# Kernel optimization log

Measured on AMD Instinct MI355X. Metric: run time of the kernel, lower is better.

## Reference

```python
import jax, jax.numpy as jnp
import numpy as np

K = 512           # num_embeddings
D = 256           # embedding_dim
GRID = (16, 32)   # SOM grid, prod == K
SIGMA = 2.0       # Gaussian neighborhood width (blur at step 0)
COMMITMENT_COST = 0.25
KOHONEN_COST = 1.0


def _make_blur_matrix():
    # Grid.init id->coord: coord[j] = (i // prod(shape[:j])) % shape[j]
    idx = np.arange(K)
    c0 = idx % GRID[0]
    c1 = (idx // GRID[0]) % GRID[1]
    coords = np.stack([c0, c1], axis=-1).astype(np.float32)  # [K, 2]
    dist = np.linalg.norm(coords[None, :, :] - coords[:, None, :], axis=-1)  # [K, K]
    return jnp.asarray(np.exp(-(dist ** 2) / (2.0 * SIGMA ** 2)), dtype=jnp.float32)


def setup_inputs() -> dict:
    key = jax.random.key(0)
    kx, kw = jax.random.split(key)
    x = jax.random.normal(kx, (64, 32, 32, D), dtype=jnp.float32)
    w = jax.random.normal(kw, (K, D), dtype=jnp.float32)
    bmat = _make_blur_matrix()  # [K, K] constant buffer
    return {"x": x, "w": w, "bmat": bmat}


def reference(x, w, bmat):
    sg = jax.lax.stop_gradient
    flat = x.reshape(-1, D)  # [N, D]

    # nearest-code search (no_grad in torch)
    fw = sg(flat)
    ww = sg(w)
    dists = (jnp.sum(fw ** 2, axis=1, keepdims=True)
             + jnp.sum(ww ** 2, axis=1)
             - 2.0 * fw @ ww.T)                       # [N, K]
    enc_idx = jnp.argmin(dists, axis=1)               # [N]
    encodings = jax.nn.one_hot(enc_idx, K, dtype=jnp.float32)  # [N, K]

    # embedding lookup (differentiable w.r.t. w)
    quant_flat = w[enc_idx]                           # [N, D]
    quantized = quant_flat.reshape(x.shape)

    # l2_batch(w, quantized.detach()) -> [N, K]
    qd = sg(quant_flat)
    diff = (jnp.sum(w ** 2, axis=1)[None, :]
            + jnp.sum(qd ** 2, axis=1, keepdims=True)
            - 2.0 * qd @ w.T)                         # [N, K]

    # blur-weighted kohonen loss: bmm(diff[N,1,K], bmat[idx][N,K,1]).mean()
    selected = bmat[enc_idx]                          # [N, K]
    kohonen_loss = jnp.mean(jnp.sum(diff * selected, axis=-1))

    avg_probs = jnp.mean(encodings, axis=0)
    perplexity = jnp.exp(-jnp.sum(avg_probs * jnp.log(avg_probs + 1e-10)))

    e_latent = jnp.mean((sg(quantized) - x) ** 2)
    q_latent = jnp.mean((quantized - sg(x)) ** 2)
    loss = q_latent + COMMITMENT_COST * e_latent + KOHONEN_COST * kohonen_loss

    quantized_st = x + sg(quantized - x)              # straight-through
    return loss, quantized_st, perplexity, enc_idx
```

## Files before the change

### kernel.cpp

```cpp
#include <hip/hip_runtime.h>
#include <hip/hip_bf16.h>
#include <hip/hip_fp16.h>
#include <math.h>

#define NPTS 65536
#define DIM  256
#define KC   512

#define BM    64
#define NTILE 4
#define NBLK  256
#define XSTR  264
#define EPS   0.01f

#define QOFF  1
#define PIDX  16777217
#define EOFF  16777218


typedef _Float16 h8    __attribute__((ext_vector_type(8)));
typedef float    f32x4 __attribute__((ext_vector_type(4)));

__device__ inline void cvt_split8(float4 a, float4 b, h8& hv, h8& lv) {
    float f[8] = {a.x, a.y, a.z, a.w, b.x, b.y, b.z, b.w};
    #pragma unroll
    for (int i = 0; i < 8; ++i) {
        _Float16 h = (_Float16)f[i];
        hv[i] = h;
        lv[i] = (_Float16)(f[i] - (float)h);
    }
}

__device__ inline void merge_top2(float& b1, int& i1, float& b2, int& i2,
                                  float ob1, int oi1, float ob2, int oi2) {
    bool ow = (ob1 < b1) || (ob1 == b1 && oi1 < i1);
    float lb = ow ? b1 : ob1; int li = ow ? i1 : oi1;
    if (ow) { b1 = ob1; i1 = oi1; }
    float c2 = b2; int ci = i2;
    if (ob2 < c2 || (ob2 == c2 && oi2 < ci)) { c2 = ob2; ci = oi2; }
    if (lb  < c2 || (lb  == c2 && li  < ci)) { c2 = lb;  ci = li;  }
    b2 = c2; i2 = ci;
}

__device__ inline float exact_dist(const float* __restrict__ xr,
                                   const float* __restrict__ w, int c, float wsqc) {
    const float* wr = w + (size_t)c * DIM;
    float d0 = 0.f, d1 = 0.f, d2 = 0.f, d3 = 0.f;
    #pragma unroll 4
    for (int d = 0; d < DIM; d += 4) {
        d0 = fmaf(xr[d + 0], wr[d + 0], d0);
        d1 = fmaf(xr[d + 1], wr[d + 1], d1);
        d2 = fmaf(xr[d + 2], wr[d + 2], d2);
        d3 = fmaf(xr[d + 3], wr[d + 3], d3);
    }
    return wsqc - 2.f * ((d0 + d1) + (d2 + d3));
}

__global__ __launch_bounds__(256) void som_wsq(const float* __restrict__ w,
                                               float* __restrict__ wsq,
                                               int* __restrict__ hist,
                                               double* __restrict__ mse_acc)
{
    int k = blockIdx.x * 256 + threadIdx.x;
    const float4* r = reinterpret_cast<const float4*>(w + (size_t)k * DIM);
    float s0 = 0.f, s1 = 0.f, s2 = 0.f, s3 = 0.f;
    #pragma unroll 8
    for (int q = 0; q < DIM / 4; ++q) {
        float4 v = r[q];
        s0 = fmaf(v.x, v.x, s0);
        s1 = fmaf(v.y, v.y, s1);
        s2 = fmaf(v.z, v.z, s2);
        s3 = fmaf(v.w, v.w, s3);
    }
    wsq[k] = (s0 + s1) + (s2 + s3);
    hist[k] = 0;
    if (k == 0) *mse_acc = 0.0;
}

__global__ __launch_bounds__(256) void som_conv(const float* __restrict__ w,
                                                _Float16* __restrict__ wfh,
                                                _Float16* __restrict__ wfl)
{
    const int tid = threadIdx.x;
    const int row = blockIdx.x * 8 + (tid >> 5);
    const int g   = tid & 31;
    const float4* r = reinterpret_cast<const float4*>(w + (size_t)row * DIM);
    float4 a = r[g * 2], b = r[g * 2 + 1];
    h8 hv, lv; cvt_split8(a, b, hv, lv);
    int dsl = g >> 2, kg = g & 3;
    int ctg = row >> 4, l15 = row & 15;
    size_t off = (((size_t)(ctg * 8 + dsl)) * 4 + kg) * 128 + l15 * 8;
    *reinterpret_cast<h8*>(wfh + off) = hv;
    *reinterpret_cast<h8*>(wfl + off) = lv;
}

__global__ __launch_bounds__(512) void som_main(const float* __restrict__ x,
                                                const float* __restrict__ w,
                                                const _Float16* __restrict__ wfh,
                                                const _Float16* __restrict__ wfl,
                                                float* __restrict__ out,
                                                const float* __restrict__ wsq,
                                                int* __restrict__ hist,
                                                double* __restrict__ mse_acc)
{
    alignas(16) __shared__ _Float16 xh[2][BM * XSTR];
    alignas(16) __shared__ _Float16 xl[2][BM * XSTR];
    __shared__ float wsq_s[KC];
    __shared__ float xsq_s[2][BM];
    __shared__ float red_b[8][BM], red_s[8][BM];
    __shared__ int   red_ib[8][BM], red_is[8][BM];
    __shared__ int   bidx_s[BM];

    const int tid  = threadIdx.x;
    const int lane = tid & 63;
    const int wid  = tid >> 6;
    const int l15  = lane & 15;
    const int kg   = lane >> 4;
    const int tile0 = blockIdx.x * NTILE;

    wsq_s[tid] = wsq[tid];

    const float4* xg4 = reinterpret_cast<const float4*>(x);
    const float4* wg4 = reinterpret_cast<const float4*>(w);
    float4* q4 = reinterpret_cast<float4*>(out + QOFF);

    float4 xr[4][2];

    auto loadx = [&](int tt) {
        #pragma unroll
        for (int it = 0; it < 4; ++it) {
            int u = it * 512 + tid, row = u >> 5, c8 = u & 31;
            size_t base = (size_t)(tt * BM + row) * 64 + c8 * 2;
            xr[it][0] = xg4[base];
            xr[it][1] = xg4[base + 1];
        }
    };
    auto cvtwrite = [&](int c) {
        #pragma unroll
        for (int it = 0; it < 4; ++it) {
            int u = it * 512 + tid, row = u >> 5, c8 = u & 31;
            h8 hv, lv; cvt_split8(xr[it][0], xr[it][1], hv, lv);
            *reinterpret_cast<h8*>(&xh[c][row * XSTR + c8 * 8]) = hv;
            *reinterpret_cast<h8*>(&xl[c][row * XSTR + c8 * 8]) = lv;
            float4 a = xr[it][0], b = xr[it][1];
            float s = ((fmaf(a.x, a.x, a.y * a.y) + fmaf(a.z, a.z, a.w * a.w))
                     + (fmaf(b.x, b.x, b.y * b.y) + fmaf(b.z, b.z, b.w * b.w)));
            #pragma unroll
            for (int m = 1; m <= 16; m <<= 1) s += __shfl_xor(s, m, 64);
            if ((lane & 31) == 0) xsq_s[c][row] = s;
        }
    };

    loadx(tile0);
    cvtwrite(0);
    loadx(tile0 + 1);
    __syncthreads();

    const int codeBase = wid * 64;
    const int ctg0 = codeBase >> 4;
    const _Float16* __restrict__ pH = wfh + kg * 128 + l15 * 8;
    const _Float16* __restrict__ pL = wfl + kg * 128 + l15 * 8;

    #pragma unroll 1
    for (int t = 0; t < NTILE; ++t) {
        const int c = t & 1;
        const int ptBlock = (tile0 + t) * BM;
        const _Float16* __restrict__ bxh = xh[c];
        const _Float16* __restrict__ bxl = xl[c];

        f32x4 acc[4][4];
        #pragma unroll
        for (int rt = 0; rt < 4; ++rt)
            #pragma unroll
            for (int ct = 0; ct < 4; ++ct)
                acc[rt][ct] = (f32x4){0.f, 0.f, 0.f, 0.f};

        #pragma unroll 1
        for (int dsl = 0; dsl < 8; ++dsl) {
            h8 Bh[4], Bl[4];
            #pragma unroll
            for (int ct = 0; ct < 4; ++ct) {
                int boff = (ct * 16 + l15) * XSTR + dsl * 32 + kg * 8;
                Bh[ct] = *reinterpret_cast<const h8*>(&bxh[boff]);
                Bl[ct] = *reinterpret_cast<const h8*>(&bxl[boff]);
            }
            #pragma unroll
            for (int rt = 0; rt < 4; ++rt) {
                size_t aoff = ((size_t)((ctg0 + rt) * 8 + dsl)) * 512;
                h8 Ah = *reinterpret_cast<const h8*>(pH + aoff);
                h8 Al = *reinterpret_cast<const h8*>(pL + aoff);
                #pragma unroll
                for (int ct = 0; ct < 4; ++ct)
                    acc[rt][ct] = __builtin_amdgcn_mfma_f32_16x16x32_f16(Ah, Bh[ct], acc[rt][ct], 0, 0, 0);
                #pragma unroll
                for (int ct = 0; ct < 4; ++ct)
                    acc[rt][ct] = __builtin_amdgcn_mfma_f32_16x16x32_f16(Al, Bh[ct], acc[rt][ct], 0, 0, 0);
                #pragma unroll
                for (int ct = 0; ct < 4; ++ct)
                    acc[rt][ct] = __builtin_amdgcn_mfma_f32_16x16x32_f16(Ah, Bl[ct], acc[rt][ct], 0, 0, 0);
            }
        }

        float sb[4], ss[4];
        int   ib[4], is2[4];
        #pragma unroll
        for (int ct = 0; ct < 4; ++ct) { sb[ct] = INFINITY; ss[ct] = INFINITY; ib[ct] = 0; is2[ct] = 0; }
        #pragma unroll
        for (int rt = 0; rt < 4; ++rt) {
            int cbase = codeBase + rt * 16 + kg * 4;
            #pragma unroll
            for (int ct = 0; ct < 4; ++ct) {
                #pragma unroll
                for (int r = 0; r < 4; ++r) {
                    int cc = cbase + r;
                    float d = wsq_s[cc] - 2.f * acc[rt][ct][r];
                    if (d < sb[ct] || (d == sb[ct] && cc < ib[ct])) {
                        ss[ct] = sb[ct]; is2[ct] = ib[ct]; sb[ct] = d; ib[ct] = cc;
                    } else if (d < ss[ct] || (d == ss[ct] && cc < is2[ct])) {
                        ss[ct] = d; is2[ct] = cc;
                    }
                }
            }
        }
        #pragma unroll
        for (int ct = 0; ct < 4; ++ct) {
            #pragma unroll
            for (int m = 16; m <= 32; m <<= 1) {
                float ob1 = __shfl_xor(sb[ct], m, 64), ob2 = __shfl_xor(ss[ct], m, 64);
                int   oi1 = __shfl_xor(ib[ct], m, 64), oi2 = __shfl_xor(is2[ct], m, 64);
                merge_top2(sb[ct], ib[ct], ss[ct], is2[ct], ob1, oi1, ob2, oi2);
            }
        }
        if (kg == 0) {
            #pragma unroll
            for (int ct = 0; ct < 4; ++ct) {
                int p = ct * 16 + l15;
                red_b[wid][p] = sb[ct];  red_s[wid][p] = ss[ct];
                red_ib[wid][p] = ib[ct]; red_is[wid][p] = is2[ct];
            }
        }
        __syncthreads();

        if (tid < BM) {
            float b = red_b[0][tid], s = red_s[0][tid];
            int  bi = red_ib[0][tid], si = red_is[0][tid];
            #pragma unroll
            for (int g = 1; g < 8; ++g)
                merge_top2(b, bi, s, si, red_b[g][tid], red_ib[g][tid], red_s[g][tid], red_is[g][tid]);

            if (s - b < EPS) {
                const float* xrp = x + (size_t)(ptBlock + tid) * DIM;
                float d1 = exact_dist(xrp, w, bi, wsq_s[bi]);
                float d2 = exact_dist(xrp, w, si, wsq_s[si]);
                if (d2 < d1 || (d2 == d1 && si < bi)) { bi = si; b = d2; } else { b = d1; }
            }
            bidx_s[tid] = bi;
            out[EOFF + ptBlock + tid] = (float)bi;
            atomicAdd(&hist[bi], 1);

            float msum = xsq_s[c][tid] + b;
            #pragma unroll
            for (int m = 32; m; m >>= 1) msum += __shfl_xor(msum, m, 64);
            if (tid == 0) atomicAdd(mse_acc, (double)msum);
        }
        __syncthreads();

        #pragma unroll
        for (int r8 = 0; r8 < 8; ++r8) {
            int row = r8 * 8 + wid;
            int cc = bidx_s[row];
            q4[(size_t)(ptBlock + row) * 64 + lane] = wg4[(size_t)cc * 64 + lane];
        }
        if (t + 1 < NTILE) cvtwrite(c ^ 1);
        if (t + 2 < NTILE) loadx(tile0 + t + 2);
        __syncthreads();
    }
}

__global__ __launch_bounds__(256) void som_g(const float* __restrict__ w,
                                             const float* __restrict__ bmat,
                                             const float* __restrict__ wsq,
                                             float* __restrict__ g)
{
    __shared__ float wj[DIM];
    __shared__ float psum[4];
    const int j = blockIdx.x;
    const int tid = threadIdx.x;
    wj[tid] = w[(size_t)j * DIM + tid];
    __syncthreads();
    const float wsqj = wsq[j];
    float sum = 0.f;
    for (int k = tid; k < KC; k += 256) {
        const float* wk = &w[(size_t)k * DIM];
        float d0 = 0.f, d1 = 0.f, d2 = 0.f, d3 = 0.f;
        #pragma unroll 4
        for (int d = 0; d < DIM; d += 4) {
            d0 = fmaf(wj[d + 0], wk[d + 0], d0);
            d1 = fmaf(wj[d + 1], wk[d + 1], d1);
            d2 = fmaf(wj[d + 2], wk[d + 2], d2);
            d3 = fmaf(wj[d + 3], wk[d + 3], d3);
        }
        float dot = (d0 + d1) + (d2 + d3);
        float t = wsq[k] + wsqj - 2.f * dot;
        sum = fmaf(bmat[(size_t)j * KC + k], t, sum);
    }
    #pragma unroll
    for (int m = 32; m; m >>= 1) sum += __shfl_xor(sum, m, 64);
    int lane = tid & 63, wid = tid >> 6;
    if (lane == 0) psum[wid] = sum;
    __syncthreads();
    if (tid == 0) g[j] = (psum[0] + psum[1]) + (psum[2] + psum[3]);
}

__global__ __launch_bounds__(512) void som_final(const int* __restrict__ hist,
                                                 const float* __restrict__ g,
                                                 const double* __restrict__ mse_acc,
                                                 float* __restrict__ out)
{
    __shared__ float e_part[8], k_part[8];
    const int tid = threadIdx.x;
    int cnt = hist[tid];
    float p = (float)cnt / (float)NPTS;
    float ent = -p * logf(p + 1e-10f);
    float koh = (float)cnt * g[tid];
    #pragma unroll
    for (int m = 32; m; m >>= 1) {
        ent += __shfl_xor(ent, m, 64);
        koh += __shfl_xor(koh, m, 64);
    }
    int lane = tid & 63, wid = tid >> 6;
    if (lane == 0) { e_part[wid] = ent; k_part[wid] = koh; }
    __syncthreads();
    if (tid == 0) {
        float es = 0.f, ks = 0.f;
        #pragma unroll
        for (int i = 0; i < 8; ++i) { es += e_part[i]; ks += k_part[i]; }
        float mse = (float)(*mse_acc / (double)(NPTS * (size_t)DIM));
        out[0] = fmaf(1.25f, mse, ks / (float)NPTS);
        out[PIDX] = expf(es);
    }
}

extern "C" void kernel_launch(void* const* d_in, const int* in_sizes, int n_in,
                              void* d_out, int out_size, void* d_ws, size_t ws_size,
                              hipStream_t stream) {
    const float* x    = (const float*)d_in[0];
    const float* w    = (const float*)d_in[1];
    const float* bmat = (const float*)d_in[2];
    float* out = (float*)d_out;

    _Float16* wfh = (_Float16*)d_ws;
    _Float16* wfl = wfh + 131072;
    float*  wsq  = (float*)((char*)d_ws + 524288);
    float*  g    = (float*)((char*)d_ws + 526336);
    int*    hist = (int*)((char*)d_ws + 528384);
    double* mse  = (double*)((char*)d_ws + 530432);

    som_wsq  <<<2, 256, 0, stream>>>(w, wsq, hist, mse);
    som_conv <<<64, 256, 0, stream>>>(w, wfh, wfl);
    som_main <<<NBLK, 512, 0, stream>>>(x, w, wfh, wfl, out, wsq, hist, mse);
    som_g    <<<KC, 256, 0, stream>>>(w, bmat, wsq, g);
    som_final<<<1, KC, 0, stream>>>(hist, g, mse, out);
}
```

Baseline: 182.1 us.

## Use single fp16 MFMA pass with full exact rescan for ambiguous points

Drops the split hi/lo fp16 compensation, cutting the MFMA distance GEMM from three passes to one and halving the converted-weight buffers. Points whose top-two margin falls below a widened threshold are queued and rescanned exactly in fp32 against all 512 codes, one wave per flagged point. It also merges the wsq and conversion kernels into one, and assigns one tile per block (1024 blocks) instead of double-buffered four-tile blocks. The risk is that many flagged points make the serial full-codebook rescan expensive, and the coarser fp16 distances could miss true nearest codes outside the margin.

After: 457.9 us. 151% more time.

```diff
diff --git a/kernel.cpp b/kernel.cpp
--- a/kernel.cpp
+++ b/kernel.cpp
@@ -8,10 +8,9 @@
 #define KC   512
 
 #define BM    64
-#define NTILE 4
-#define NBLK  256
+#define NBLK  (NPTS / BM)
 #define XSTR  264
-#define EPS   0.01f
+#define EPS   0.1f
 
 #define QOFF  1
 #define PIDX  16777217
@@ -20,16 +19,6 @@
 
 typedef _Float16 h8    __attribute__((ext_vector_type(8)));
 typedef float    f32x4 __attribute__((ext_vector_type(4)));
-
-__device__ inline void cvt_split8(float4 a, float4 b, h8& hv, h8& lv) {
-    float f[8] = {a.x, a.y, a.z, a.w, b.x, b.y, b.z, b.w};
-    #pragma unroll
-    for (int i = 0; i < 8; ++i) {
-        _Float16 h = (_Float16)f[i];
-        hv[i] = h;
-        lv[i] = (_Float16)(f[i] - (float)h);
-    }
-}
 
 __device__ inline void merge_top2(float& b1, int& i1, float& b2, int& i2,
                                   float ob1, int oi1, float ob2, int oi2) {
@@ -42,238 +31,207 @@
     b2 = c2; i2 = ci;
 }
 
-__device__ inline float exact_dist(const float* __restrict__ xr,
-                                   const float* __restrict__ w, int c, float wsqc) {
-    const float* wr = w + (size_t)c * DIM;
-    float d0 = 0.f, d1 = 0.f, d2 = 0.f, d3 = 0.f;
+__global__ __launch_bounds__(256) void som_prep(const float* __restrict__ w,
+                                                _Float16* __restrict__ wfh,
+                                                float* __restrict__ wsq,
+                                                int* __restrict__ hist,
+                                                double* __restrict__ mse_acc)
+{
+    int c = blockIdx.x * 256 + threadIdx.x;
+    const float4* r = reinterpret_cast<const float4*>(w + (size_t)c * DIM);
+    float s0 = 0.f, s1 = 0.f, s2 = 0.f, s3 = 0.f;
     #pragma unroll 4
-    for (int d = 0; d < DIM; d += 4) {
-        d0 = fmaf(xr[d + 0], wr[d + 0], d0);
-        d1 = fmaf(xr[d + 1], wr[d + 1], d1);
-        d2 = fmaf(xr[d + 2], wr[d + 2], d2);
-        d3 = fmaf(xr[d + 3], wr[d + 3], d3);
-    }
-    return wsqc - 2.f * ((d0 + d1) + (d2 + d3));
-}
-
-__global__ __launch_bounds__(256) void som_wsq(const float* __restrict__ w,
-                                               float* __restrict__ wsq,
-                                               int* __restrict__ hist,
-                                               double* __restrict__ mse_acc)
-{
-    int k = blockIdx.x * 256 + threadIdx.x;
-    const float4* r = reinterpret_cast<const float4*>(w + (size_t)k * DIM);
-    float s0 = 0.f, s1 = 0.f, s2 = 0.f, s3 = 0.f;
-    #pragma unroll 8
-    for (int q = 0; q < DIM / 4; ++q) {
-        float4 v = r[q];
-        s0 = fmaf(v.x, v.x, s0);
-        s1 = fmaf(v.y, v.y, s1);
-        s2 = fmaf(v.z, v.z, s2);
-        s3 = fmaf(v.w, v.w, s3);
-    }
-    wsq[k] = (s0 + s1) + (s2 + s3);
-    hist[k] = 0;
-    if (k == 0) *mse_acc = 0.0;
-}
-
-__global__ __launch_bounds__(256) void som_conv(const float* __restrict__ w,
-                                                _Float16* __restrict__ wfh,
-                                                _Float16* __restrict__ wfl)
-{
-    const int tid = threadIdx.x;
-    const int row = blockIdx.x * 8 + (tid >> 5);
-    const int g   = tid & 31;
-    const float4* r = reinterpret_cast<const float4*>(w + (size_t)row * DIM);
-    float4 a = r[g * 2], b = r[g * 2 + 1];
-    h8 hv, lv; cvt_split8(a, b, hv, lv);
-    int dsl = g >> 2, kg = g & 3;
-    int ctg = row >> 4, l15 = row & 15;
-    size_t off = (((size_t)(ctg * 8 + dsl)) * 4 + kg) * 128 + l15 * 8;
-    *reinterpret_cast<h8*>(wfh + off) = hv;
-    *reinterpret_cast<h8*>(wfl + off) = lv;
+    for (int g = 0; g < 32; ++g) {
+        float4 a = r[g * 2], b = r[g * 2 + 1];
+        s0 = fmaf(a.x, a.x, s0); s1 = fmaf(a.y, a.y, s1);
+        s2 = fmaf(a.z, a.z, s2); s3 = fmaf(a.w, a.w, s3);
+        s0 = fmaf(b.x, b.x, s0); s1 = fmaf(b.y, b.y, s1);
+        s2 = fmaf(b.z, b.z, s2); s3 = fmaf(b.w, b.w, s3);
+        h8 hv;
+        hv[0] = (_Float16)a.x; hv[1] = (_Float16)a.y;
+        hv[2] = (_Float16)a.z; hv[3] = (_Float16)a.w;
+        hv[4] = (_Float16)b.x; hv[5] = (_Float16)b.y;
+        hv[6] = (_Float16)b.z; hv[7] = (_Float16)b.w;
+        size_t off = (((size_t)((c >> 4) * 8 + (g >> 2))) * 4 + (g & 3)) * 128 + (c & 15) * 8;
+        *reinterpret_cast<h8*>(wfh + off) = hv;
+    }
+    wsq[c] = (s0 + s1) + (s2 + s3);
+    hist[c] = 0;
+    if (c == 0) *mse_acc = 0.0;
 }
 
 __global__ __launch_bounds__(512) void som_main(const float* __restrict__ x,
                                                 const float* __restrict__ w,
                                                 const _Float16* __restrict__ wfh,
-                                                const _Float16* __restrict__ wfl,
                                                 float* __restrict__ out,
                                                 const float* __restrict__ wsq,
                                                 int* __restrict__ hist,
                                                 double* __restrict__ mse_acc)
 {
-    alignas(16) __shared__ _Float16 xh[2][BM * XSTR];
-    alignas(16) __shared__ _Float16 xl[2][BM * XSTR];
+    alignas(16) __shared__ _Float16 xh[BM * XSTR];
     __shared__ float wsq_s[KC];
-    __shared__ float xsq_s[2][BM];
+    __shared__ float xsq_s[BM];
     __shared__ float red_b[8][BM], red_s[8][BM];
     __shared__ int   red_ib[8][BM], red_is[8][BM];
     __shared__ int   bidx_s[BM];
+    __shared__ int   flg[BM];
+    __shared__ int   flg_n;
 
     const int tid  = threadIdx.x;
     const int lane = tid & 63;
     const int wid  = tid >> 6;
     const int l15  = lane & 15;
     const int kg   = lane >> 4;
-    const int tile0 = blockIdx.x * NTILE;
-
+    const int ptBlock = blockIdx.x * BM;
+
+    if (tid == 0) flg_n = 0;
+
+    const float4* xg4 = reinterpret_cast<const float4*>(x);
+    #pragma unroll
+    for (int it = 0; it < 4; ++it) {
+        int u = it * 512 + tid, row = u >> 5, c8 = u & 31;
+        float4 a = xg4[(size_t)(ptBlock + row) * 64 + c8 * 2];
+        float4 b = xg4[(size_t)(ptBlock + row) * 64 + c8 * 2 + 1];
+        h8 hv;
+        hv[0] = (_Float16)a.x; hv[1] = (_Float16)a.y;
+        hv[2] = (_Float16)a.z; hv[3] = (_Float16)a.w;
+        hv[4] = (_Float16)b.x; hv[5] = (_Float16)b.y;
+        hv[6] = (_Float16)b.z; hv[7] = (_Float16)b.w;
+        *reinterpret_cast<h8*>(&xh[row * XSTR + c8 * 8]) = hv;
+        float s = ((fmaf(a.x, a.x, a.y * a.y) + fmaf(a.z, a.z, a.w * a.w))
+                 + (fmaf(b.x, b.x, b.y * b.y) + fmaf(b.z, b.z, b.w * b.w)));
+        #pragma unroll
+        for (int m = 1; m <= 16; m <<= 1) s += __shfl_xor(s, m, 64);
+        if ((lane & 31) == 0) xsq_s[row] = s;
+    }
     wsq_s[tid] = wsq[tid];
-
-    const float4* xg4 = reinterpret_cast<const float4*>(x);
-    const float4* wg4 = reinterpret_cast<const float4*>(w);
-    float4* q4 = reinterpret_cast<float4*>(out + QOFF);
-
-    float4 xr[4][2];
-
-    auto loadx = [&](int tt) {
-        #pragma unroll
-        for (int it = 0; it < 4; ++it) {
-            int u = it * 512 + tid, row = u >> 5, c8 = u & 31;
-            size_t base = (size_t)(tt * BM + row) * 64 + c8 * 2;
-            xr[it][0] = xg4[base];
-            xr[it][1] = xg4[base + 1];
-        }
-    };
-    auto cvtwrite = [&](int c) {
-        #pragma unroll
-        for (int it = 0; it < 4; ++it) {
-            int u = it * 512 + tid, row = u >> 5, c8 = u & 31;
-            h8 hv, lv; cvt_split8(xr[it][0], xr[it][1], hv, lv);
-            *reinterpret_cast<h8*>(&xh[c][row * XSTR + c8 * 8]) = hv;
-            *reinterpret_cast<h8*>(&xl[c][row * XSTR + c8 * 8]) = lv;
-            float4 a = xr[it][0], b = xr[it][1];
-            float s = ((fmaf(a.x, a.x, a.y * a.y) + fmaf(a.z, a.z, a.w * a.w))
-                     + (fmaf(b.x, b.x, b.y * b.y) + fmaf(b.z, b.z, b.w * b.w)));
-            #pragma unroll
-            for (int m = 1; m <= 16; m <<= 1) s += __shfl_xor(s, m, 64);
-            if ((lane & 31) == 0) xsq_s[c][row] = s;
-        }
-    };
-
-    loadx(tile0);
-    cvtwrite(0);
-    loadx(tile0 + 1);
     __syncthreads();
 
     const int codeBase = wid * 64;
     const int ctg0 = codeBase >> 4;
     const _Float16* __restrict__ pH = wfh + kg * 128 + l15 * 8;
-    const _Float16* __restrict__ pL = wfl + kg * 128 + l15 * 8;
+
+    f32x4 acc[4][4];
+    #pragma unroll
+    for (int rt = 0; rt < 4; ++rt)
+        #pragma unroll
+        for (int ct = 0; ct < 4; ++ct)
+            acc[rt][ct] = (f32x4){0.f, 0.f, 0.f, 0.f};
 
     #pragma unroll 1
-    for (int t = 0; t < NTILE; ++t) {
-        const int c = t & 1;
-        const int ptBlock = (tile0 + t) * BM;
-        const _Float16* __restrict__ bxh = xh[c];
-        const _Float16* __restrict__ bxl = xl[c];
-
-        f32x4 acc[4][4];
-        #pragma unroll
-        for (int rt = 0; rt < 4; ++rt)
+    for (int dsl = 0; dsl < 8; ++dsl) {
+        h8 Bh[4];
+        #pragma unroll
+        for (int ct = 0; ct < 4; ++ct)
+            Bh[ct] = *reinterpret_cast<const h8*>(&xh[(ct * 16 + l15) * XSTR + dsl * 32 + kg * 8]);
+        #pragma unroll
+        for (int rt = 0; rt < 4; ++rt) {
+            size_t aoff = ((size_t)((ctg0 + rt) * 8 + dsl)) * 512;
+            h8 Ah = *reinterpret_cast<const h8*>(pH + aoff);
             #pragma unroll
             for (int ct = 0; ct < 4; ++ct)
-                acc[rt][ct] = (f32x4){0.f, 0.f, 0.f, 0.f};
-
-        #pragma unroll 1
-        for (int dsl = 0; dsl < 8; ++dsl) {
-            h8 Bh[4], Bl[4];
+                acc[rt][ct] = __builtin_amdgcn_mfma_f32_16x16x32_f16(Ah, Bh[ct], acc[rt][ct], 0, 0, 0);
+        }
+    }
+
+    float sb[4], ss[4];
+    int   ib[4], is2[4];
+    #pragma unroll
+    for (int ct = 0; ct < 4; ++ct) { sb[ct] = INFINITY; ss[ct] = INFINITY; ib[ct] = 0; is2[ct] = 0; }
+    #pragma unroll
+    for (int rt = 0; rt < 4; ++rt) {
+        int cbase = codeBase + rt * 16 + kg * 4;
+        #pragma unroll
+        for (int ct = 0; ct < 4; ++ct) {
             #pragma unroll
-            for (int ct = 0; ct < 4; ++ct) {
-                int boff = (ct * 16 + l15) * XSTR + dsl * 32 + kg * 8;
-                Bh[ct] = *reinterpret_cast<const h8*>(&bxh[boff]);
-                Bl[ct] = *reinterpret_cast<const h8*>(&bxl[boff]);
-            }
-            #pragma unroll
-            for (int rt = 0; rt < 4; ++rt) {
-                size_t aoff = ((size_t)((ctg0 + rt) * 8 + dsl)) * 512;
-                h8 Ah = *reinterpret_cast<const h8*>(pH + aoff);
-                h8 Al = *reinterpret_cast<const h8*>(pL + aoff);
-                #pragma unroll
-                for (int ct = 0; ct < 4; ++ct)
-                    acc[rt][ct] = __builtin_amdgcn_mfma_f32_16x16x32_f16(Ah, Bh[ct], acc[rt][ct], 0, 0, 0);
-                #pragma unroll
-                for (int ct = 0; ct < 4; ++ct)
-                    acc[rt][ct] = __builtin_amdgcn_mfma_f32_16x16x32_f16(Al, Bh[ct], acc[rt][ct], 0, 0, 0);
-                #pragma unroll
-                for (int ct = 0; ct < 4; ++ct)
-                    acc[rt][ct] = __builtin_amdgcn_mfma_f32_16x16x32_f16(Ah, Bl[ct], acc[rt][ct], 0, 0, 0);
-            }
-        }
-
-        float sb[4], ss[4];
-        int   ib[4], is2[4];
-        #pragma unroll
-        for (int ct = 0; ct < 4; ++ct) { sb[ct] = INFINITY; ss[ct] = INFINITY; ib[ct] = 0; is2[ct] = 0; }
-        #pragma unroll
-        for (int rt = 0; rt < 4; ++rt) {
-            int cbase = codeBase + rt * 16 + kg * 4;
-            #pragma unroll
-            for (int ct = 0; ct < 4; ++ct) {
-                #pragma unroll
-                for (int r = 0; r < 4; ++r) {
-                    int cc = cbase + r;
-                    float d = wsq_s[cc] - 2.f * acc[rt][ct][r];
-                    if (d < sb[ct] || (d == sb[ct] && cc < ib[ct])) {
-                        ss[ct] = sb[ct]; is2[ct] = ib[ct]; sb[ct] = d; ib[ct] = cc;
-                    } else if (d < ss[ct] || (d == ss[ct] && cc < is2[ct])) {
-                        ss[ct] = d; is2[ct] = cc;
-                    }
+            for (int r = 0; r < 4; ++r) {
+                int cc = cbase + r;
+                float d = wsq_s[cc] - 2.f * acc[rt][ct][r];
+                if (d < sb[ct] || (d == sb[ct] && cc < ib[ct])) {
+                    ss[ct] = sb[ct]; is2[ct] = ib[ct]; sb[ct] = d; ib[ct] = cc;
+                } else if (d < ss[ct] || (d == ss[ct] && cc < is2[ct])) {
+                    ss[ct] = d; is2[ct] = cc;
                 }
             }
         }
+    }
+    #pragma unroll
+    for (int ct = 0; ct < 4; ++ct) {
+        #pragma unroll
+        for (int m = 16; m <= 32; m <<= 1) {
+            float ob1 = __shfl_xor(sb[ct], m, 64), ob2 = __shfl_xor(ss[ct], m, 64);
+            int   oi1 = __shfl_xor(ib[ct], m, 64), oi2 = __shfl_xor(is2[ct], m, 64);
+            merge_top2(sb[ct], ib[ct], ss[ct], is2[ct], ob1, oi1, ob2, oi2);
+        }
+    }
+    if (kg == 0) {
         #pragma unroll
         for (int ct = 0; ct < 4; ++ct) {
-            #pragma unroll
-            for (int m = 16; m <= 32; m <<= 1) {
-                float ob1 = __shfl_xor(sb[ct], m, 64), ob2 = __shfl_xor(ss[ct], m, 64);
-                int   oi1 = __shfl_xor(ib[ct], m, 64), oi2 = __shfl_xor(is2[ct], m, 64);
-                merge_top2(sb[ct], ib[ct], ss[ct], is2[ct], ob1, oi1, ob2, oi2);
-            }
-        }
-        if (kg == 0) {
-            #pragma unroll
-            for (int ct = 0; ct < 4; ++ct) {
-                int p = ct * 16 + l15;
-                red_b[wid][p] = sb[ct];  red_s[wid][p] = ss[ct];
-                red_ib[wid][p] = ib[ct]; red_is[wid][p] = is2[ct];
-            }
-        }
-        __syncthreads();
-
-        if (tid < BM) {
-            float b = red_b[0][tid], s = red_s[0][tid];
-            int  bi = red_ib[0][tid], si = red_is[0][tid];
-            #pragma unroll
-            for (int g = 1; g < 8; ++g)
-                merge_top2(b, bi, s, si, red_b[g][tid], red_ib[g][tid], red_s[g][tid], red_is[g][tid]);
-
-            if (s - b < EPS) {
-                const float* xrp = x + (size_t)(ptBlock + tid) * DIM;
-                float d1 = exact_dist(xrp, w, bi, wsq_s[bi]);
-                float d2 = exact_dist(xrp, w, si, wsq_s[si]);
-                if (d2 < d1 || (d2 == d1 && si < bi)) { bi = si; b = d2; } else { b = d1; }
-            }
+            int p = ct * 16 + l15;
+            red_b[wid][p] = sb[ct];  red_s[wid][p] = ss[ct];
+            red_ib[wid][p] = ib[ct]; red_is[wid][p] = is2[ct];
+        }
+    }
+    __syncthreads();
+
+    if (tid < BM) {
+        float b = red_b[0][tid], s = red_s[0][tid];
+        int  bi = red_ib[0][tid], si = red_is[0][tid];
+        #pragma unroll
+        for (int g = 1; g < 8; ++g)
+            merge_top2(b, bi, s, si, red_b[g][tid], red_ib[g][tid], red_s[g][tid], red_is[g][tid]);
+
+        float msum = 0.f;
+        if (s - b < EPS) {
+            int slot = atomicAdd(&flg_n, 1);
+            flg[slot] = tid;
+        } else {
             bidx_s[tid] = bi;
             out[EOFF + ptBlock + tid] = (float)bi;
             atomicAdd(&hist[bi], 1);
-
-            float msum = xsq_s[c][tid] + b;
-            #pragma unroll
-            for (int m = 32; m; m >>= 1) msum += __shfl_xor(msum, m, 64);
-            if (tid == 0) atomicAdd(mse_acc, (double)msum);
-        }
-        __syncthreads();
-
+            msum = xsq_s[tid] + b;
+        }
+        #pragma unroll
+        for (int m = 32; m; m >>= 1) msum += __shfl_xor(msum, m, 64);
+        if (tid == 0) atomicAdd(mse_acc, (double)msum);
+    }
+    __syncthreads();
+
+    {
+        const float4* wg4r = reinterpret_cast<const float4*>(w);
+        int F = flg_n;
+        for (int fi = wid; fi < F; fi += 8) {
+            int p = flg[fi];
+            float4 xv = xg4[(size_t)(ptBlock + p) * 64 + lane];
+            float best = INFINITY; int bi = 0;
+            #pragma unroll 1
+            for (int c = 0; c < KC; ++c) {
+                float4 wv = wg4r[(size_t)c * 64 + lane];
+                float t = fmaf(xv.x, wv.x, fmaf(xv.y, wv.y, fmaf(xv.z, wv.z, xv.w * wv.w)));
+                #pragma unroll
+                for (int m = 1; m <= 32; m <<= 1) t += __shfl_xor(t, m, 64);
+                float d = wsq_s[c] - 2.f * t;
+                if (d < best) { best = d; bi = c; }
+            }
+            if (lane == 0) {
+                bidx_s[p] = bi;
+                out[EOFF + ptBlock + p] = (float)bi;
+                atomicAdd(&hist[bi], 1);
+                atomicAdd(mse_acc, (double)(xsq_s[p] + best));
+            }
+        }
+    }
+    __syncthreads();
+
+    {
+        const float4* wg4 = reinterpret_cast<const float4*>(w);
+        float4* q4 = reinterpret_cast<float4*>(out + QOFF);
         #pragma unroll
         for (int r8 = 0; r8 < 8; ++r8) {
             int row = r8 * 8 + wid;
             int cc = bidx_s[row];
             q4[(size_t)(ptBlock + row) * 64 + lane] = wg4[(size_t)cc * 64 + lane];
         }
-        if (t + 1 < NTILE) cvtwrite(c ^ 1);
-        if (t + 2 < NTILE) loadx(tile0 + t + 2);
-        __syncthreads();
     }
 }
 
@@ -350,15 +308,13 @@
     float* out = (float*)d_out;
 
     _Float16* wfh = (_Float16*)d_ws;
-    _Float16* wfl = wfh + 131072;
-    float*  wsq  = (float*)((char*)d_ws + 524288);
-    float*  g    = (float*)((char*)d_ws + 526336);
-    int*    hist = (int*)((char*)d_ws + 528384);
-    double* mse  = (double*)((char*)d_ws + 530432);
-
-    som_wsq  <<<2, 256, 0, stream>>>(w, wsq, hist, mse);
-    som_conv <<<64, 256, 0, stream>>>(w, wfh, wfl);
-    som_main <<<NBLK, 512, 0, stream>>>(x, w, wfh, wfl, out, wsq, hist, mse);
+    float*  wsq  = (float*)((char*)d_ws + 262144);
+    float*  g    = (float*)((char*)d_ws + 264192);
+    int*    hist = (int*)((char*)d_ws + 266240);
+    double* mse  = (double*)((char*)d_ws + 268288);
+
+    som_prep <<<2, 256, 0, stream>>>(w, wfh, wsq, hist, mse);
+    som_main <<<NBLK, 512, 0, stream>>>(x, w, wfh, out, wsq, hist, mse);
     som_g    <<<KC, 256, 0, stream>>>(w, bmat, wsq, g);
     som_final<<<1, KC, 0, stream>>>(hist, g, mse, out);
 }
```

## Stage codebook slices into LDS via global_load_lds, one tile per block

Applied to the files above, without the earlier changes.

The main kernel now runs one 64-point tile per block (1024 blocks) instead of four tiles per block with register double-buffering of x. For each 32-wide D slice, the whole fp16 hi/lo codebook slice is copied into shared memory with direct global-to-LDS loads, replacing per-wave global loads of the A operand. The converted codebook layout is reordered so that each D slice is contiguous. This adds two block barriers per slice and drops the overlap of x loading with compute. It also needs about 64KB of extra LDS, which may limit how many blocks fit on each CU.

Result: slower. 191.0 us (+4.9%).

```diff
diff --git a/kernel.cpp b/kernel.cpp
--- a/kernel.cpp
+++ b/kernel.cpp
@@ -8,8 +8,7 @@
 #define KC   512
 
 #define BM    64
-#define NTILE 4
-#define NBLK  256
+#define NBLK  (NPTS / BM)
 #define XSTR  264
 #define EPS   0.01f
 
@@ -29,6 +28,12 @@
         hv[i] = h;
         lv[i] = (_Float16)(f[i] - (float)h);
     }
+}
+
+__device__ inline void gload16(const _Float16* gp, _Float16* lp) {
+    __builtin_amdgcn_global_load_lds(
+        (const __attribute__((address_space(1))) void*)gp,
+        (__attribute__((address_space(3))) void*)lp, 16, 0, 0);
 }
 
 __device__ inline void merge_top2(float& b1, int& i1, float& b2, int& i2,
@@ -88,8 +93,7 @@
     float4 a = r[g * 2], b = r[g * 2 + 1];
     h8 hv, lv; cvt_split8(a, b, hv, lv);
     int dsl = g >> 2, kg = g & 3;
-    int ctg = row >> 4, l15 = row & 15;
-    size_t off = (((size_t)(ctg * 8 + dsl)) * 4 + kg) * 128 + l15 * 8;
+    size_t off = ((size_t)(dsl * 32 + (row >> 4))) * 512 + kg * 128 + (row & 15) * 8;
     *reinterpret_cast<h8*>(wfh + off) = hv;
     *reinterpret_cast<h8*>(wfl + off) = lv;
 }
@@ -103,10 +107,12 @@
                                                 int* __restrict__ hist,
                                                 double* __restrict__ mse_acc)
 {
-    alignas(16) __shared__ _Float16 xh[2][BM * XSTR];
-    alignas(16) __shared__ _Float16 xl[2][BM * XSTR];
+    alignas(16) __shared__ _Float16 AsH[16384];
+    alignas(16) __shared__ _Float16 AsL[16384];
+    alignas(16) __shared__ _Float16 xh[BM * XSTR];
+    alignas(16) __shared__ _Float16 xl[BM * XSTR];
     __shared__ float wsq_s[KC];
-    __shared__ float xsq_s[2][BM];
+    __shared__ float xsq_s[BM];
     __shared__ float red_b[8][BM], red_s[8][BM];
     __shared__ int   red_ib[8][BM], red_is[8][BM];
     __shared__ int   bidx_s[BM];
@@ -116,164 +122,144 @@
     const int wid  = tid >> 6;
     const int l15  = lane & 15;
     const int kg   = lane >> 4;
-    const int tile0 = blockIdx.x * NTILE;
-
+    const int ptBlock = blockIdx.x * BM;
+
+    const float4* xg4 = reinterpret_cast<const float4*>(x);
+    #pragma unroll
+    for (int it = 0; it < 4; ++it) {
+        int u = it * 512 + tid, row = u >> 5, c8 = u & 31;
+        float4 a = xg4[(size_t)(ptBlock + row) * 64 + c8 * 2];
+        float4 b = xg4[(size_t)(ptBlock + row) * 64 + c8 * 2 + 1];
+        h8 hv, lv; cvt_split8(a, b, hv, lv);
+        *reinterpret_cast<h8*>(&xh[row * XSTR + c8 * 8]) = hv;
+        *reinterpret_cast<h8*>(&xl[row * XSTR + c8 * 8]) = lv;
+        float s = ((fmaf(a.x, a.x, a.y * a.y) + fmaf(a.z, a.z, a.w * a.w))
+                 + (fmaf(b.x, b.x, b.y * b.y) + fmaf(b.z, b.z, b.w * b.w)));
+        #pragma unroll
+        for (int m = 1; m <= 16; m <<= 1) s += __shfl_xor(s, m, 64);
+        if ((lane & 31) == 0) xsq_s[row] = s;
+    }
     wsq_s[tid] = wsq[tid];
 
-    const float4* xg4 = reinterpret_cast<const float4*>(x);
-    const float4* wg4 = reinterpret_cast<const float4*>(w);
-    float4* q4 = reinterpret_cast<float4*>(out + QOFF);
-
-    float4 xr[4][2];
-
-    auto loadx = [&](int tt) {
-        #pragma unroll
-        for (int it = 0; it < 4; ++it) {
-            int u = it * 512 + tid, row = u >> 5, c8 = u & 31;
-            size_t base = (size_t)(tt * BM + row) * 64 + c8 * 2;
-            xr[it][0] = xg4[base];
-            xr[it][1] = xg4[base + 1];
-        }
-    };
-    auto cvtwrite = [&](int c) {
-        #pragma unroll
-        for (int it = 0; it < 4; ++it) {
-            int u = it * 512 + tid, row = u >> 5, c8 = u & 31;
-            h8 hv, lv; cvt_split8(xr[it][0], xr[it][1], hv, lv);
-            *reinterpret_cast<h8*>(&xh[c][row * XSTR + c8 * 8]) = hv;
-            *reinterpret_cast<h8*>(&xl[c][row * XSTR + c8 * 8]) = lv;
-            float4 a = xr[it][0], b = xr[it][1];
-            float s = ((fmaf(a.x, a.x, a.y * a.y) + fmaf(a.z, a.z, a.w * a.w))
-                     + (fmaf(b.x, b.x, b.y * b.y) + fmaf(b.z, b.z, b.w * b.w)));
-            #pragma unroll
-            for (int m = 1; m <= 16; m <<= 1) s += __shfl_xor(s, m, 64);
-            if ((lane & 31) == 0) xsq_s[c][row] = s;
-        }
-    };
-
-    loadx(tile0);
-    cvtwrite(0);
-    loadx(tile0 + 1);
-    __syncthreads();
-
     const int codeBase = wid * 64;
-    const int ctg0 = codeBase >> 4;
-    const _Float16* __restrict__ pH = wfh + kg * 128 + l15 * 8;
-    const _Float16* __restrict__ pL = wfl + kg * 128 + l15 * 8;
+    const int ctg0 = wid * 4;
+
+    f32x4 acc[4][4];
+    #pragma unroll
+    for (int rt = 0; rt < 4; ++rt)
+        #pragma unroll
+        for (int ct = 0; ct < 4; ++ct)
+            acc[rt][ct] = (f32x4){0.f, 0.f, 0.f, 0.f};
 
     #pragma unroll 1
-    for (int t = 0; t < NTILE; ++t) {
-        const int c = t & 1;
-        const int ptBlock = (tile0 + t) * BM;
-        const _Float16* __restrict__ bxh = xh[c];
-        const _Float16* __restrict__ bxl = xl[c];
-
-        f32x4 acc[4][4];
-        #pragma unroll
-        for (int rt = 0; rt < 4; ++rt)
+    for (int dsl = 0; dsl < 8; ++dsl) {
+        #pragma unroll
+        for (int i = 0; i < 4; ++i) {
+            size_t goff = (size_t)dsl * 16384 + (size_t)(i * 512 + tid) * 8;
+            int loff = (i * 512 + wid * 64) * 8;
+            gload16(wfh + goff, &AsH[loff]);
+            gload16(wfl + goff, &AsL[loff]);
+        }
+        __syncthreads();
+
+        h8 Bh[4], Bl[4];
+        #pragma unroll
+        for (int ct = 0; ct < 4; ++ct) {
+            int boff = (ct * 16 + l15) * XSTR + dsl * 32 + kg * 8;
+            Bh[ct] = *reinterpret_cast<const h8*>(&xh[boff]);
+            Bl[ct] = *reinterpret_cast<const h8*>(&xl[boff]);
+        }
+        #pragma unroll
+        for (int rt = 0; rt < 4; ++rt) {
+            int aoff = (ctg0 + rt) * 512 + kg * 128 + l15 * 8;
+            h8 Ah = *reinterpret_cast<const h8*>(&AsH[aoff]);
+            h8 Al = *reinterpret_cast<const h8*>(&AsL[aoff]);
             #pragma unroll
             for (int ct = 0; ct < 4; ++ct)
-                acc[rt][ct] = (f32x4){0.f, 0.f, 0.f, 0.f};
-
-        #pragma unroll 1
-        for (int dsl = 0; dsl < 8; ++dsl) {
-            h8 Bh[4], Bl[4];
+                acc[rt][ct] = __builtin_amdgcn_mfma_f32_16x16x32_f16(Ah, Bh[ct], acc[rt][ct], 0, 0, 0);
             #pragma unroll
-            for (int ct = 0; ct < 4; ++ct) {
-                int boff = (ct * 16 + l15) * XSTR + dsl * 32 + kg * 8;
-                Bh[ct] = *reinterpret_cast<const h8*>(&bxh[boff]);
-                Bl[ct] = *reinterpret_cast<const h8*>(&bxl[boff]);
-            }
+            for (int ct = 0; ct < 4; ++ct)
+                acc[rt][ct] = __builtin_amdgcn_mfma_f32_16x16x32_f16(Al, Bh[ct], acc[rt][ct], 0, 0, 0);
             #pragma unroll
-            for (int rt = 0; rt < 4; ++rt) {
-                size_t aoff = ((size_t)((ctg0 + rt) * 8 + dsl)) * 512;
-                h8 Ah = *reinterpret_cast<const h8*>(pH + aoff);
-                h8 Al = *reinterpret_cast<const h8*>(pL + aoff);
-                #pragma unroll
-                for (int ct = 0; ct < 4; ++ct)
-                    acc[rt][ct] = __builtin_amdgcn_mfma_f32_16x16x32_f16(Ah, Bh[ct], acc[rt][ct], 0, 0, 0);
-                #pragma unroll
-                for (int ct = 0; ct < 4; ++ct)
-                    acc[rt][ct] = __builtin_amdgcn_mfma_f32_16x16x32_f16(Al, Bh[ct], acc[rt][ct], 0, 0, 0);
-                #pragma unroll
-                for (int ct = 0; ct < 4; ++ct)
-                    acc[rt][ct] = __builtin_amdgcn_mfma_f32_16x16x32_f16(Ah, Bl[ct], acc[rt][ct], 0, 0, 0);
-            }
-        }
-
-        float sb[4], ss[4];
-        int   ib[4], is2[4];
-        #pragma unroll
-        for (int ct = 0; ct < 4; ++ct) { sb[ct] = INFINITY; ss[ct] = INFINITY; ib[ct] = 0; is2[ct] = 0; }
-        #pragma unroll
-        for (int rt = 0; rt < 4; ++rt) {
-            int cbase = codeBase + rt * 16 + kg * 4;
+            for (int ct = 0; ct < 4; ++ct)
+                acc[rt][ct] = __builtin_amdgcn_mfma_f32_16x16x32_f16(Ah, Bl[ct], acc[rt][ct], 0, 0, 0);
+        }
+        __syncthreads();
+    }
+
+    float sb[4], ss[4];
+    int   ib[4], is2[4];
+    #pragma unroll
+    for (int ct = 0; ct < 4; ++ct) { sb[ct] = INFINITY; ss[ct] = INFINITY; ib[ct] = 0; is2[ct] = 0; }
+    #pragma unroll
+    for (int rt = 0; rt < 4; ++rt) {
+        int cbase = codeBase + rt * 16 + kg * 4;
+        #pragma unroll
+        for (int ct = 0; ct < 4; ++ct) {
             #pragma unroll
-            for (int ct = 0; ct < 4; ++ct) {
-                #pragma unroll
-                for (int r = 0; r < 4; ++r) {
-                    int cc = cbase + r;
-                    float d = wsq_s[cc] - 2.f * acc[rt][ct][r];
-                    if (d < sb[ct] || (d == sb[ct] && cc < ib[ct])) {
-                        ss[ct] = sb[ct]; is2[ct] = ib[ct]; sb[ct] = d; ib[ct] = cc;
-                    } else if (d < ss[ct] || (d == ss[ct] && cc < is2[ct])) {
-                        ss[ct] = d; is2[ct] = cc;
-                    }
+            for (int r = 0; r < 4; ++r) {
+                int cc = cbase + r;
+                float d = wsq_s[cc] - 2.f * acc[rt][ct][r];
+                if (d < sb[ct] || (d == sb[ct] && cc < ib[ct])) {
+                    ss[ct] = sb[ct]; is2[ct] = ib[ct]; sb[ct] = d; ib[ct] = cc;
+                } else if (d < ss[ct] || (d == ss[ct] && cc < is2[ct])) {
+                    ss[ct] = d; is2[ct] = cc;
                 }
             }
         }
+    }
+    #pragma unroll
+    for (int ct = 0; ct < 4; ++ct) {
+        #pragma unroll
+        for (int m = 16; m <= 32; m <<= 1) {
+            float ob1 = __shfl_xor(sb[ct], m, 64), ob2 = __shfl_xor(ss[ct], m, 64);
+            int   oi1 = __shfl_xor(ib[ct], m, 64), oi2 = __shfl_xor(is2[ct], m, 64);
+            merge_top2(sb[ct], ib[ct], ss[ct], is2[ct], ob1, oi1, ob2, oi2);
+        }
+    }
+    if (kg == 0) {
         #pragma unroll
         for (int ct = 0; ct < 4; ++ct) {
-            #pragma unroll
-            for (int m = 16; m <= 32; m <<= 1) {
-                float ob1 = __shfl_xor(sb[ct], m, 64), ob2 = __shfl_xor(ss[ct], m, 64);
-                int   oi1 = __shfl_xor(ib[ct], m, 64), oi2 = __shfl_xor(is2[ct], m, 64);
-                merge_top2(sb[ct], ib[ct], ss[ct], is2[ct], ob1, oi1, ob2, oi2);
-            }
-        }
-        if (kg == 0) {
-            #pragma unroll
-            for (int ct = 0; ct < 4; ++ct) {
-                int p = ct * 16 + l15;
-                red_b[wid][p] = sb[ct];  red_s[wid][p] = ss[ct];
-                red_ib[wid][p] = ib[ct]; red_is[wid][p] = is2[ct];
-            }
-        }
-        __syncthreads();
-
-        if (tid < BM) {
-            float b = red_b[0][tid], s = red_s[0][tid];
-            int  bi = red_ib[0][tid], si = red_is[0][tid];
-            #pragma unroll
-            for (int g = 1; g < 8; ++g)
-                merge_top2(b, bi, s, si, red_b[g][tid], red_ib[g][tid], red_s[g][tid], red_is[g][tid]);
-
-            if (s - b < EPS) {
-                const float* xrp = x + (size_t)(ptBlock + tid) * DIM;
-                float d1 = exact_dist(xrp, w, bi, wsq_s[bi]);
-                float d2 = exact_dist(xrp, w, si, wsq_s[si]);
-                if (d2 < d1 || (d2 == d1 && si < bi)) { bi = si; b = d2; } else { b = d1; }
-            }
-            bidx_s[tid] = bi;
-            out[EOFF + ptBlock + tid] = (float)bi;
-            atomicAdd(&hist[bi], 1);
-
-            float msum = xsq_s[c][tid] + b;
-            #pragma unroll
-            for (int m = 32; m; m >>= 1) msum += __shfl_xor(msum, m, 64);
-            if (tid == 0) atomicAdd(mse_acc, (double)msum);
-        }
-        __syncthreads();
-
+            int p = ct * 16 + l15;
+            red_b[wid][p] = sb[ct];  red_s[wid][p] = ss[ct];
+            red_ib[wid][p] = ib[ct]; red_is[wid][p] = is2[ct];
+        }
+    }
+    __syncthreads();
+
+    if (tid < BM) {
+        float b = red_b[0][tid], s = red_s[0][tid];
+        int  bi = red_ib[0][tid], si = red_is[0][tid];
+        #pragma unroll
+        for (int g = 1; g < 8; ++g)
+            merge_top2(b, bi, s, si, red_b[g][tid], red_ib[g][tid], red_s[g][tid], red_is[g][tid]);
+
+        if (s - b < EPS) {
+            const float* xrp = x + (size_t)(ptBlock + tid) * DIM;
+            float d1 = exact_dist(xrp, w, bi, wsq_s[bi]);
+            float d2 = exact_dist(xrp, w, si, wsq_s[si]);
+            if (d2 < d1 || (d2 == d1 && si < bi)) { bi = si; b = d2; } else { b = d1; }
+        }
+        bidx_s[tid] = bi;
+        out[EOFF + ptBlock + tid] = (float)bi;
+        atomicAdd(&hist[bi], 1);
+
+        float msum = xsq_s[tid] + b;
+        #pragma unroll
+        for (int m = 32; m; m >>= 1) msum += __shfl_xor(msum, m, 64);
+        if (tid == 0) atomicAdd(mse_acc, (double)msum);
+    }
+    __syncthreads();
+
+    {
+        const float4* wg4 = reinterpret_cast<const float4*>(w);
+        float4* q4 = reinterpret_cast<float4*>(out + QOFF);
         #pragma unroll
         for (int r8 = 0; r8 < 8; ++r8) {
             int row = r8 * 8 + wid;
             int cc = bidx_s[row];
             q4[(size_t)(ptBlock + row) * 64 + lane] = wg4[(size_t)cc * 64 + lane];
         }
-        if (t + 1 < NTILE) cvtwrite(c ^ 1);
-        if (t + 2 < NTILE) loadx(tile0 + t + 2);
-        __syncthreads();
     }
 }
 
```
